# Performance work log

Hardware: AMD Instinct MI355X
Metric: run time of the kernel (lower is better)

The kernel has to match this reference:

```python
import jax, jax.numpy as jnp
import numpy as np

MARGIN = 0.3
EPS = 1e-6  # torch TripletMarginLoss pairwise_distance eps


def setup_inputs() -> dict:
    key = jax.random.key(0)
    k1, k2 = jax.random.split(key)
    n, d = 8192, 128
    inputs = jax.random.normal(k1, (n, d), dtype=jnp.float32)
    similarity = jax.random.randint(k2, (n, n), 0, 2, dtype=jnp.int32)
    return {"inputs": inputs, "similarity": similarity}


def reference(inputs, similarity):
    # mask[i, j] = True if j is a positive of anchor i
    mask = similarity != 0                      # (n, n) bool
    maskf = mask.astype(inputs.dtype)
    counts = maskf.sum(axis=1, keepdims=True)   # (n, 1), >0 by construction
    # per-anchor center = mean of its positives (masked mean as a GEMM)
    centers = (maskf @ inputs) / counts         # (n, d)
    # dist[i, j] = ||centers[i] - inputs[j]||_2 via the expansion trick
    # (avoids materializing the (n, n, d) difference tensor of the original)
    c2 = jnp.sum(centers * centers, axis=1)[:, None]
    x2 = jnp.sum(inputs * inputs, axis=1)[None, :]
    d2 = c2 + x2 - 2.0 * (centers @ inputs.T)
    dist = jnp.sqrt(jnp.maximum(d2, 0.0))       # (n, n)
    # dist only feeds argmin in the original (indices carry no grad)
    dist = jax.lax.stop_gradient(dist)
    # hard-negative mining: argmin of dist over negatives of each anchor
    neg_idx = jnp.argmin(jnp.where(mask, jnp.inf, dist), axis=1)  # (n,)
    neg_min = inputs[neg_idx]                   # (n, d)
    # TripletMarginLoss(margin=0.3, p=2): anchor=centers, pos=inputs, neg=neg_min
    d_ap = jnp.linalg.norm(centers - inputs + EPS, axis=1)
    d_an = jnp.linalg.norm(centers - neg_min + EPS, axis=1)
    return jnp.mean(jnp.maximum(d_ap - d_an + MARGIN, 0.0))
```

## Files before the change

kernel.cpp:

```cpp
#include <hip/hip_runtime.h>
#include <stdint.h>

#define NN 8192
#define DD 128

typedef float f32x4 __attribute__((ext_vector_type(4)));
typedef short bf16x8 __attribute__((ext_vector_type(8)));

union B8 { uint32_t u[4]; bf16x8 v; };

__device__ inline uint16_t f2bf(float f) {
  uint32_t u = __builtin_bit_cast(uint32_t, f);
  uint32_t r = (u + 0x7FFFu + ((u >> 16) & 1u)) >> 16;
  return (uint16_t)r;
}

__device__ inline f32x4 mfma16(bf16x8 a, bf16x8 b, f32x4 c) {
  return __builtin_amdgcn_mfma_f32_16x16x32_bf16(a, b, c, 0, 0, 0);
}

__device__ inline void gl_lds16(const uint16_t* g, uint16_t* l) {
  __builtin_amdgcn_global_load_lds((const __attribute__((address_space(1))) void*)g,
                                   (__attribute__((address_space(3))) void*)l, 16, 0, 0);
}

__global__ __launch_bounds__(256, 2) void k_prep_bitgen(const float* __restrict__ inp,
                                                        const int* __restrict__ sim,
                                                        uint16_t* __restrict__ inp_bf,
                                                        uint16_t* __restrict__ inpT_bf,
                                                        float* __restrict__ x2p,
                                                        uint32_t* __restrict__ bmT,
                                                        uint32_t* __restrict__ negkey,
                                                        uint32_t* __restrict__ sem,
                                                        float* __restrict__ out) {
  __shared__ uint32_t shmem[4416];
  const int tid = threadIdx.x;
  const int bid = blockIdx.x;
  if (bid < 128) {
    uint16_t* ldsT = (uint16_t*)shmem;
    float* ldsS = (float*)(shmem + 4160);
    const int gid = bid * 256 + tid;
    if (gid < NN) negkey[gid] = 0xFFFFFFFFu;
    if (gid < 64) sem[gid] = 0u;
    if (gid == 0) out[0] = 0.f;
    const int j0 = bid * 64;
    const int r = tid >> 2;
    const int dseg = (tid & 3) * 32;
    float ss = 0.f;
#pragma unroll
    for (int it = 0; it < 8; ++it) {
      float4 v = *(const float4*)(inp + (size_t)(j0 + r) * DD + dseg + it * 4);
      ss += v.x * v.x + v.y * v.y + v.z * v.z + v.w * v.w;
      uint16_t b0 = f2bf(v.x), b1 = f2bf(v.y), b2 = f2bf(v.z), b3 = f2bf(v.w);
      *(ushort4*)(inp_bf + (size_t)(j0 + r) * DD + dseg + it * 4) = make_ushort4(b0, b1, b2, b3);
      int d = dseg + it * 4;
      ldsT[(d + 0) * 65 + r] = b0;
      ldsT[(d + 1) * 65 + r] = b1;
      ldsT[(d + 2) * 65 + r] = b2;
      ldsT[(d + 3) * 65 + r] = b3;
    }
    ldsS[tid] = ss;
    __syncthreads();
    if (tid < 64)
      x2p[j0 + tid] = ldsS[tid * 4] + ldsS[tid * 4 + 1] + ldsS[tid * 4 + 2] + ldsS[tid * 4 + 3] + 512.0f;
#pragma unroll
    for (int it = 0; it < 32; ++it) {
      int flat = it * 256 + tid;
      int d = flat >> 6, jl = flat & 63;
      inpT_bf[(size_t)d * NN + j0 + jl] = ldsT[d * 65 + jl];
    }
  } else {
    uint32_t* ldsW = shmem;
    const int bx = bid - 128;
    const int lane = tid & 63, w = tid >> 6;
    const int m0 = (bx & 127) * 64;
    const int c0 = (bx >> 7) * 2048;
    int va[32], vb[32];
    {
      const int* p = sim + (size_t)(m0 + w) * NN + c0 + lane;
#pragma unroll
      for (int s = 0; s < 32; ++s) va[s] = p[s * 64];
    }
#pragma unroll 1
    for (int rr = 0; rr < 16; ++rr) {
      const int rl = rr * 4 + w;
      if (rr < 15) {
        const int* p = sim + (size_t)(m0 + rl + 4) * NN + c0 + lane;
#pragma unroll
        for (int s = 0; s < 32; ++s) vb[s] = p[s * 64];
      }
#pragma unroll
      for (int s = 0; s < 32; ++s) {
        unsigned long long ball = __ballot(va[s] != 0);
        if ((lane & 31) == 0)
          ldsW[(s * 2 + (lane >> 5)) * 64 + rl] = (uint32_t)(ball >> (lane & 32));
      }
#pragma unroll
      for (int s = 0; s < 32; ++s) va[s] = vb[s];
    }
    __syncthreads();
#pragma unroll
    for (int it = 0; it < 16; ++it) {
      int idx = it * 256 + tid;
      int kw = idx >> 6, r = idx & 63;
      bmT[(size_t)((c0 >> 5) + kw) * NN + m0 + r] = ldsW[idx];
    }
  }
}

__global__ __launch_bounds__(256, 2) void k_gemm1(const uint16_t* __restrict__ inpT,
                                                  const uint32_t* __restrict__ bmT,
                                                  float* __restrict__ part,
                                                  uint32_t* __restrict__ sem,
                                                  float* __restrict__ centers,
                                                  uint16_t* __restrict__ cen_bf) {
  __shared__ __align__(16) uint16_t ldsB[2][128 * 64];
  __shared__ float sInv[128];
  __shared__ uint32_t s_done;
  const int tid = threadIdx.x, lane = tid & 63, w = tid >> 6;
  const int col = lane & 15, quad = lane >> 4;
  const int m0 = blockIdx.x * 128;
  const int kb0 = blockIdx.y * 1024;
  const int wm = (w >> 1) * 64, wn = (w & 1) * 64;
  const int swz = (col & 7) << 4;
  f32x4 acc[4][4];
  const f32x4 z = {0.f, 0.f, 0.f, 0.f};
#pragma unroll
  for (int r = 0; r < 4; ++r)
#pragma unroll
    for (int c = 0; c < 4; ++c) acc[r][c] = z;

  uint32_t mwA[8], mwB[8];
  const int srow = lane >> 3;
  const int schk = (lane & 7) ^ (srow & 7);

#define STAGE3(BUF, KB)                                                                       \
  {                                                                                           \
    _Pragma("unroll") for (int c = 0; c < 4; ++c) {                                           \
      const uint16_t* gsrc =                                                                  \
          inpT + (size_t)(w * 32 + c * 8 + srow) * NN + (KB) + (schk << 3);                   \
      gl_lds16(gsrc, &ldsB[BUF][(w * 32 + c * 8) * 64]);                                      \
    }                                                                                         \
  }

#define LDM3(MW, KB)                                                                          \
  {                                                                                           \
    _Pragma("unroll") for (int rr = 0; rr < 4; ++rr)                                          \
      _Pragma("unroll") for (int h = 0; h < 2; ++h)                                           \
        MW[rr * 2 + h] = bmT[(size_t)(((KB) >> 5) + h) * NN + m0 + wm + rr * 16 + col];       \
  }

#define COMP3(BUF, MW)                                                                        \
  {                                                                                           \
    _Pragma("unroll") for (int h = 0; h < 2; ++h) {                                           \
      B8 af[4];                                                                               \
      _Pragma("unroll") for (int rr = 0; rr < 4; ++rr) {                                      \
        uint32_t word = MW[rr * 2 + h];                                                       \
        uint32_t b = (word >> (quad * 8)) & 0xFFu;                                            \
        uint32_t s = b * 0x8001u;                                                             \
        _Pragma("unroll") for (int p = 0; p < 4; ++p)                                         \
          af[rr].u[p] = ((s >> (2 * p)) & 0x10001u) * 0x3F80u;                                \
      }                                                                                       \
      const int eoff = ((h * 64 + quad * 16) ^ swz) >> 1;                                     \
      _Pragma("unroll") for (int cc = 0; cc < 4; ++cc) {                                      \
        bf16x8 bfr = *(const bf16x8*)(&ldsB[BUF][(wn + cc * 16 + col) * 64 + eoff]);          \
        _Pragma("unroll") for (int rr = 0; rr < 4; ++rr)                                      \
          acc[rr][cc] = mfma16(af[rr].v, bfr, acc[rr][cc]);                                   \
      }                                                                                       \
    }                                                                                         \
  }

  STAGE3(0, kb0);
  LDM3(mwA, kb0);
  __syncthreads();
#pragma unroll 1
  for (int ks = 0; ks < 16; ks += 2) {
    const int kb = kb0 + ks * 64;
    STAGE3(1, kb + 64);
    LDM3(mwB, kb + 64);
    COMP3(0, mwA);
    __syncthreads();
    if (ks + 2 < 16) {
      STAGE3(0, kb + 128);
      LDM3(mwA, kb + 128);
    }
    COMP3(1, mwB);
    __syncthreads();
  }
#undef STAGE3
#undef LDM3
#undef COMP3

  float* pp = part + (size_t)blockIdx.y * NN * DD;
#pragma unroll
  for (int rr = 0; rr < 4; ++rr)
#pragma unroll
    for (int cc = 0; cc < 4; ++cc)
#pragma unroll
      for (int g = 0; g < 4; ++g)
        pp[(size_t)(m0 + wm + rr * 16 + quad * 4 + g) * DD + wn + cc * 16 + col] = acc[rr][cc][g];

  __threadfence();
  __syncthreads();
  if (tid == 0) s_done = atomicAdd(&sem[blockIdx.x], 1u);
  __syncthreads();
  if (s_done != 7u) return;
  __threadfence();

  if (tid < 128) {
    uint32_t cnt = 0;
#pragma unroll 4
    for (int kw = 0; kw < 256; ++kw) cnt += __popc(bmT[(size_t)kw * NN + m0 + tid]);
    sInv[tid] = 1.0f / (float)cnt;
  }
  __syncthreads();

#pragma unroll 1
  for (int it = 0; it < 16; ++it) {
    const int f4 = it * 256 + tid;
    const int row = f4 >> 5;
    const int c4 = (f4 & 31) * 4;
    const size_t idx = (size_t)(m0 + row) * DD + c4;
    float4 v = *(const float4*)(part + idx);
#pragma unroll
    for (int s = 1; s < 8; ++s) {
      float4 u = *(const float4*)(part + (size_t)s * NN * DD + idx);
      v.x += u.x; v.y += u.y; v.z += u.z; v.w += u.w;
    }
    const float inv = sInv[row];
    v.x *= inv; v.y *= inv; v.z *= inv; v.w *= inv;
    *(float4*)(centers + idx) = v;
    *(ushort4*)(cen_bf + idx) = make_ushort4(f2bf(v.x), f2bf(v.y), f2bf(v.z), f2bf(v.w));
  }
}

__global__ __launch_bounds__(256, 2) void k_argmin(const uint16_t* __restrict__ cen_bf,
                                                   const uint16_t* __restrict__ inp_bf,
                                                   const uint32_t* __restrict__ bmT,
                                                   const float* __restrict__ x2p,
                                                   uint32_t* __restrict__ negkey) {
  __shared__ __align__(16) uint16_t ldsX[2][64 * 128];
  const int tid = threadIdx.x, lane = tid & 63, w = tid >> 6;
  const int col = lane & 15, quad = lane >> 4;
  const int i0 = blockIdx.x * 128;
  const int jbase = blockIdx.y * 1024;
  const int wi = w * 32;
  const int swz = (col & 7) << 4;

  bf16x8 af[2][4];
#pragma unroll
  for (int rr = 0; rr < 2; ++rr)
#pragma unroll
    for (int kk = 0; kk < 4; ++kk)
      af[rr][kk] = *(const bf16x8*)(cen_bf + (size_t)(i0 + wi + rr * 16 + col) * DD + kk * 32 + quad * 8);

  uint32_t best[2][4];
#pragma unroll
  for (int rr = 0; rr < 2; ++rr)
#pragma unroll
    for (int g = 0; g < 4; ++g) best[rr][g] = 0xFFFFFFFFu;

  const f32x4 z = {0.f, 0.f, 0.f, 0.f};
  const int srow = lane >> 4;

#define STAGE5(BUF, J0)                                                                       \
  {                                                                                           \
    _Pragma("unroll") for (int c = 0; c < 4; ++c) {                                           \
      const int r7 = (c * 4 + srow) & 7;                                                      \
      const uint16_t* gsrc =                                                                  \
          inp_bf + (size_t)((J0) + w * 16 + c * 4 + srow) * DD + (((lane & 15) ^ r7) << 3);   \
      gl_lds16(gsrc, &ldsX[BUF][(w * 16 + c * 4) * 128]);                                     \
    }                                                                                         \
  }

#define COMP5(BUF, J0)                                                                        \
  {                                                                                           \
    uint32_t mw[2][2][4];                                                                     \
    float xv[4];                                                                              \
    _Pragma("unroll") for (int h = 0; h < 2; ++h)                                             \
      _Pragma("unroll") for (int rr = 0; rr < 2; ++rr)                                        \
        _Pragma("unroll") for (int g = 0; g < 4; ++g)                                         \
          mw[h][rr][g] =                                                                      \
              bmT[(size_t)(((J0) >> 5) + h) * NN + i0 + wi + rr * 16 + quad * 4 + g];         \
    _Pragma("unroll") for (int cc = 0; cc < 4; ++cc) xv[cc] = x2p[(J0) + cc * 16 + col];      \
    f32x4 acc[2][4];                                                                          \
    _Pragma("unroll") for (int rr = 0; rr < 2; ++rr)                                          \
      _Pragma("unroll") for (int cc = 0; cc < 4; ++cc) acc[rr][cc] = z;                       \
    _Pragma("unroll") for (int kk = 0; kk < 4; ++kk) {                                        \
      const int eoff = ((kk * 64 + quad * 16) ^ swz) >> 1;                                    \
      _Pragma("unroll") for (int cc = 0; cc < 4; ++cc) {                                      \
        bf16x8 b = *(const bf16x8*)(&ldsX[BUF][(cc * 16 + col) * 128 + eoff]);                \
        acc[0][cc] = mfma16(af[0][kk], b, acc[0][cc]);                                        \
        acc[1][cc] = mfma16(af[1][kk], b, acc[1][cc]);                                        \
      }                                                                                       \
    }                                                                                         \
    _Pragma("unroll") for (int cc = 0; cc < 4; ++cc) {                                        \
      const int jj = cc * 16 + col;                                                           \
      const float xq = xv[cc];                                                                \
      const uint32_t jpre = (uint32_t)((J0) + jj);                                            \
      const int sh = 31 - ((cc & 1) * 16 + col);                                              \
      _Pragma("unroll") for (int rr = 0; rr < 2; ++rr)                                        \
        _Pragma("unroll") for (int g = 0; g < 4; ++g) {                                       \
          float v = fmaf(-2.0f, acc[rr][cc][g], xq);                                          \
          uint32_t u = __builtin_bit_cast(uint32_t, v);                                       \
          uint32_t key = (u & 0xFFFFE000u) | jpre;                                            \
          key |= (mw[cc >> 1][rr][g] << sh) & 0x80000000u;                                    \
          best[rr][g] = min(best[rr][g], key);                                                \
        }                                                                                     \
    }                                                                                         \
  }

  STAGE5(0, jbase);
  __syncthreads();
#pragma unroll 1
  for (int st = 0; st < 16; st += 2) {
    const int j0 = jbase + st * 64;
    STAGE5(1, j0 + 64);
    COMP5(0, j0);
    __syncthreads();
    if (st + 2 < 16) STAGE5(0, j0 + 128);
    COMP5(1, j0 + 64);
    __syncthreads();
  }
#undef STAGE5
#undef COMP5

#pragma unroll
  for (int rr = 0; rr < 2; ++rr)
#pragma unroll
    for (int g = 0; g < 4; ++g) {
      uint32_t k = best[rr][g];
#pragma unroll
      for (int d = 1; d < 16; d <<= 1) {
        uint32_t o = (uint32_t)__shfl_xor((int)k, d);
        k = min(k, o);
      }
      if (col == 0) atomicMin(&negkey[i0 + wi + rr * 16 + quad * 4 + g], k);
    }
}

__global__ __launch_bounds__(256) void k_loss(const float* __restrict__ centers,
                                              const float* __restrict__ inp,
                                              const uint32_t* __restrict__ negkey,
                                              float* __restrict__ out) {
  __shared__ float lds[4];
  const int tid = threadIdx.x, lane = tid & 63, w = tid >> 6;
  float local = 0.f;
#pragma unroll 1
  for (int a = 0; a < 4; ++a) {
    int i = blockIdx.x * 16 + w * 4 + a;
    float2 c = *(const float2*)(centers + (size_t)i * DD + lane * 2);
    float2 x = *(const float2*)(inp + (size_t)i * DD + lane * 2);
    uint32_t ni = negkey[i] & (NN - 1);
    float2 gv = *(const float2*)(inp + (size_t)ni * DD + lane * 2);
    float e0 = c.x - x.x + 1e-6f, e1 = c.y - x.y + 1e-6f;
    float f0 = c.x - gv.x + 1e-6f, f1 = c.y - gv.y + 1e-6f;
    float dap = e0 * e0 + e1 * e1;
    float dan = f0 * f0 + f1 * f1;
#pragma unroll
    for (int d = 32; d; d >>= 1) {
      dap += __shfl_down(dap, d);
      dan += __shfl_down(dan, d);
    }
    if (lane == 0) local += fmaxf(sqrtf(dap) - sqrtf(dan) + 0.3f, 0.f);
  }
  if (lane == 0) lds[w] = local;
  __syncthreads();
  if (tid == 0) atomicAdd(out, (lds[0] + lds[1] + lds[2] + lds[3]) * (1.0f / 8192.0f));
}

extern "C" void kernel_launch(void* const* d_in, const int* in_sizes, int n_in,
                              void* d_out, int out_size, void* d_ws, size_t ws_size,
                              hipStream_t stream) {
  (void)in_sizes; (void)n_in; (void)out_size; (void)ws_size;
  const float* inp = (const float*)d_in[0];
  const int* sim = (const int*)d_in[1];
  float* out = (float*)d_out;
  char* ws = (char*)d_ws;

  uint32_t* bmT     = (uint32_t*)ws;
  float* part       = (float*)(ws + (8u << 20));
  float* centers    = (float*)(ws + (40u << 20));
  uint16_t* inp_bf  = (uint16_t*)(ws + (44u << 20));
  uint16_t* inpT_bf = (uint16_t*)(ws + (46u << 20));
  uint16_t* cen_bf  = (uint16_t*)(ws + (48u << 20));
  float* x2p        = (float*)(ws + (50u << 20));
  uint32_t* sem     = (uint32_t*)(ws + (50u << 20) + 32768u);
  uint32_t* negkey  = (uint32_t*)(ws + (50u << 20) + 65536u);

  k_prep_bitgen<<<640, 256, 0, stream>>>(inp, sim, inp_bf, inpT_bf, x2p, bmT, negkey, sem, out);
  k_gemm1<<<dim3(64, 8), 256, 0, stream>>>(inpT_bf, bmT, part, sem, centers, cen_bf);
  k_argmin<<<dim3(64, 8), 256, 0, stream>>>(cen_bf, inp_bf, bmT, x2p, negkey);
  k_loss<<<512, 256, 0, stream>>>(centers, inp, negkey, out);
}
```

Before: 518.6 us.

## Fuse all stages into one persistent kernel with software grid barriers

Merges the prep/bitgen, masked GEMM, center reduction, argmin and loss kernels into a single 512-block kernel separated by atomic-counter grid barriers. Per-row positive counts are now gathered with popcount atomics during bitmask generation, and the reduction of the partial center sums is spread across all blocks instead of only the last block per row tile. The aim is to remove kernel launch gaps and the serialized tail reduction. In exchange it adds spin-wait barrier cost and two memset launches, and it depends on all 512 blocks being co-resident (2 per CU) to avoid deadlock.

```diff
diff --git a/kernel.cpp b/kernel.cpp
--- a/kernel.cpp
+++ b/kernel.cpp
@@ -3,6 +3,7 @@
 
 #define NN 8192
 #define DD 128
+#define GRID 512
 
 typedef float f32x4 __attribute__((ext_vector_type(4)));
 typedef short bf16x8 __attribute__((ext_vector_type(8)));
@@ -24,24 +25,41 @@
                                    (__attribute__((address_space(3))) void*)l, 16, 0, 0);
 }
 
-__global__ __launch_bounds__(256, 2) void k_prep_bitgen(const float* __restrict__ inp,
-                                                        const int* __restrict__ sim,
-                                                        uint16_t* __restrict__ inp_bf,
-                                                        uint16_t* __restrict__ inpT_bf,
-                                                        float* __restrict__ x2p,
-                                                        uint32_t* __restrict__ bmT,
-                                                        uint32_t* __restrict__ negkey,
-                                                        uint32_t* __restrict__ sem,
-                                                        float* __restrict__ out) {
-  __shared__ uint32_t shmem[4416];
+__device__ inline void gbar(uint32_t* cnt, uint32_t tgt) {
+  __syncthreads();
+  __threadfence();
+  if (threadIdx.x == 0) {
+    atomicAdd(cnt, 1u);
+    while (atomicAdd(cnt, 0u) < tgt) __builtin_amdgcn_s_sleep(8);
+  }
+  __syncthreads();
+  __threadfence();
+}
+
+__global__ __launch_bounds__(256, 2) void k_mega(const float* __restrict__ inp,
+                                                 const int* __restrict__ sim,
+                                                 uint16_t* __restrict__ inp_bf,
+                                                 uint16_t* __restrict__ inpT_bf,
+                                                 float* __restrict__ x2p,
+                                                 uint32_t* __restrict__ bmT,
+                                                 uint32_t* __restrict__ counts,
+                                                 float* __restrict__ part,
+                                                 float* __restrict__ centers,
+                                                 uint16_t* __restrict__ cen_bf,
+                                                 uint32_t* __restrict__ negkey,
+                                                 float* __restrict__ out,
+                                                 uint32_t* __restrict__ bar) {
+  __shared__ __align__(16) uint8_t smem[32768];
   const int tid = threadIdx.x;
   const int bid = blockIdx.x;
+  const int lane = tid & 63, w = tid >> 6;
+  const int col = lane & 15, quad = lane >> 4;
+
   if (bid < 128) {
-    uint16_t* ldsT = (uint16_t*)shmem;
-    float* ldsS = (float*)(shmem + 4160);
+    uint16_t* ldsT = (uint16_t*)smem;
+    float* ldsS = (float*)(smem + 16640);
     const int gid = bid * 256 + tid;
     if (gid < NN) negkey[gid] = 0xFFFFFFFFu;
-    if (gid < 64) sem[gid] = 0u;
     if (gid == 0) out[0] = 0.f;
     const int j0 = bid * 64;
     const int r = tid >> 2;
@@ -69,12 +87,12 @@
       int d = flat >> 6, jl = flat & 63;
       inpT_bf[(size_t)d * NN + j0 + jl] = ldsT[d * 65 + jl];
     }
-  } else {
-    uint32_t* ldsW = shmem;
-    const int bx = bid - 128;
-    const int lane = tid & 63, w = tid >> 6;
-    const int m0 = (bx & 127) * 64;
-    const int c0 = (bx >> 7) * 2048;
+    __syncthreads();
+  }
+  {
+    uint32_t* ldsW = (uint32_t*)smem;
+    const int m0 = (bid & 127) * 64;
+    const int c0 = (bid >> 7) * 2048;
     int va[32], vb[32];
     {
       const int* p = sim + (size_t)(m0 + w) * NN + c0 + lane;
@@ -89,12 +107,15 @@
 #pragma unroll
         for (int s = 0; s < 32; ++s) vb[s] = p[s * 64];
       }
+      uint32_t cnt = 0;
 #pragma unroll
       for (int s = 0; s < 32; ++s) {
         unsigned long long ball = __ballot(va[s] != 0);
+        cnt += (uint32_t)__popcll(ball);
         if ((lane & 31) == 0)
           ldsW[(s * 2 + (lane >> 5)) * 64 + rl] = (uint32_t)(ball >> (lane & 32));
       }
+      if (lane == 0) atomicAdd(&counts[m0 + rl], cnt);
 #pragma unroll
       for (int s = 0; s < 32; ++s) va[s] = vb[s];
     }
@@ -106,39 +127,31 @@
       bmT[(size_t)((c0 >> 5) + kw) * NN + m0 + r] = ldsW[idx];
     }
   }
-}
-
-__global__ __launch_bounds__(256, 2) void k_gemm1(const uint16_t* __restrict__ inpT,
-                                                  const uint32_t* __restrict__ bmT,
-                                                  float* __restrict__ part,
-                                                  uint32_t* __restrict__ sem,
-                                                  float* __restrict__ centers,
-                                                  uint16_t* __restrict__ cen_bf) {
-  __shared__ __align__(16) uint16_t ldsB[2][128 * 64];
-  __shared__ float sInv[128];
-  __shared__ uint32_t s_done;
-  const int tid = threadIdx.x, lane = tid & 63, w = tid >> 6;
-  const int col = lane & 15, quad = lane >> 4;
-  const int m0 = blockIdx.x * 128;
-  const int kb0 = blockIdx.y * 1024;
-  const int wm = (w >> 1) * 64, wn = (w & 1) * 64;
-  const int swz = (col & 7) << 4;
-  f32x4 acc[4][4];
-  const f32x4 z = {0.f, 0.f, 0.f, 0.f};
-#pragma unroll
-  for (int r = 0; r < 4; ++r)
-#pragma unroll
-    for (int c = 0; c < 4; ++c) acc[r][c] = z;
-
-  uint32_t mwA[8], mwB[8];
-  const int srow = lane >> 3;
-  const int schk = (lane & 7) ^ (srow & 7);
+  gbar(bar, 1 * GRID);
+
+  {
+    uint16_t (*ldsB)[128 * 64] = (uint16_t(*)[128 * 64])smem;
+    const int bx = bid & 63, by = bid >> 6;
+    const int m0 = bx * 128;
+    const int kb0 = by * 1024;
+    const int wm = (w >> 1) * 64, wn = (w & 1) * 64;
+    const int swz = (col & 7) << 4;
+    f32x4 acc[4][4];
+    const f32x4 z = {0.f, 0.f, 0.f, 0.f};
+#pragma unroll
+    for (int r = 0; r < 4; ++r)
+#pragma unroll
+      for (int c = 0; c < 4; ++c) acc[r][c] = z;
+
+    uint32_t mwA[8], mwB[8];
+    const int srow = lane >> 3;
+    const int schk = (lane & 7) ^ (srow & 7);
 
 #define STAGE3(BUF, KB)                                                                       \
   {                                                                                           \
     _Pragma("unroll") for (int c = 0; c < 4; ++c) {                                           \
       const uint16_t* gsrc =                                                                  \
-          inpT + (size_t)(w * 32 + c * 8 + srow) * NN + (KB) + (schk << 3);                   \
+          inpT_bf + (size_t)(w * 32 + c * 8 + srow) * NN + (KB) + (schk << 3);                \
       gl_lds16(gsrc, &ldsB[BUF][(w * 32 + c * 8) * 64]);                                      \
     }                                                                                         \
   }
@@ -170,98 +183,81 @@
     }                                                                                         \
   }
 
-  STAGE3(0, kb0);
-  LDM3(mwA, kb0);
-  __syncthreads();
-#pragma unroll 1
-  for (int ks = 0; ks < 16; ks += 2) {
-    const int kb = kb0 + ks * 64;
-    STAGE3(1, kb + 64);
-    LDM3(mwB, kb + 64);
-    COMP3(0, mwA);
-    __syncthreads();
-    if (ks + 2 < 16) {
-      STAGE3(0, kb + 128);
-      LDM3(mwA, kb + 128);
-    }
-    COMP3(1, mwB);
-    __syncthreads();
-  }
+    STAGE3(0, kb0);
+    LDM3(mwA, kb0);
+    __syncthreads();
+#pragma unroll 1
+    for (int ks = 0; ks < 16; ks += 2) {
+      const int kb = kb0 + ks * 64;
+      STAGE3(1, kb + 64);
+      LDM3(mwB, kb + 64);
+      COMP3(0, mwA);
+      __syncthreads();
+      if (ks + 2 < 16) {
+        STAGE3(0, kb + 128);
+        LDM3(mwA, kb + 128);
+      }
+      COMP3(1, mwB);
+      __syncthreads();
+    }
 #undef STAGE3
 #undef LDM3
 #undef COMP3
 
-  float* pp = part + (size_t)blockIdx.y * NN * DD;
-#pragma unroll
-  for (int rr = 0; rr < 4; ++rr)
-#pragma unroll
-    for (int cc = 0; cc < 4; ++cc)
-#pragma unroll
-      for (int g = 0; g < 4; ++g)
-        pp[(size_t)(m0 + wm + rr * 16 + quad * 4 + g) * DD + wn + cc * 16 + col] = acc[rr][cc][g];
-
-  __threadfence();
-  __syncthreads();
-  if (tid == 0) s_done = atomicAdd(&sem[blockIdx.x], 1u);
-  __syncthreads();
-  if (s_done != 7u) return;
-  __threadfence();
-
-  if (tid < 128) {
-    uint32_t cnt = 0;
-#pragma unroll 4
-    for (int kw = 0; kw < 256; ++kw) cnt += __popc(bmT[(size_t)kw * NN + m0 + tid]);
-    sInv[tid] = 1.0f / (float)cnt;
-  }
-  __syncthreads();
-
-#pragma unroll 1
-  for (int it = 0; it < 16; ++it) {
-    const int f4 = it * 256 + tid;
-    const int row = f4 >> 5;
-    const int c4 = (f4 & 31) * 4;
-    const size_t idx = (size_t)(m0 + row) * DD + c4;
-    float4 v = *(const float4*)(part + idx);
-#pragma unroll
-    for (int s = 1; s < 8; ++s) {
-      float4 u = *(const float4*)(part + (size_t)s * NN * DD + idx);
-      v.x += u.x; v.y += u.y; v.z += u.z; v.w += u.w;
-    }
-    const float inv = sInv[row];
-    v.x *= inv; v.y *= inv; v.z *= inv; v.w *= inv;
-    *(float4*)(centers + idx) = v;
-    *(ushort4*)(cen_bf + idx) = make_ushort4(f2bf(v.x), f2bf(v.y), f2bf(v.z), f2bf(v.w));
-  }
-}
-
-__global__ __launch_bounds__(256, 2) void k_argmin(const uint16_t* __restrict__ cen_bf,
-                                                   const uint16_t* __restrict__ inp_bf,
-                                                   const uint32_t* __restrict__ bmT,
-                                                   const float* __restrict__ x2p,
-                                                   uint32_t* __restrict__ negkey) {
-  __shared__ __align__(16) uint16_t ldsX[2][64 * 128];
-  const int tid = threadIdx.x, lane = tid & 63, w = tid >> 6;
-  const int col = lane & 15, quad = lane >> 4;
-  const int i0 = blockIdx.x * 128;
-  const int jbase = blockIdx.y * 1024;
-  const int wi = w * 32;
-  const int swz = (col & 7) << 4;
-
-  bf16x8 af[2][4];
-#pragma unroll
-  for (int rr = 0; rr < 2; ++rr)
-#pragma unroll
-    for (int kk = 0; kk < 4; ++kk)
-      af[rr][kk] = *(const bf16x8*)(cen_bf + (size_t)(i0 + wi + rr * 16 + col) * DD + kk * 32 + quad * 8);
-
-  uint32_t best[2][4];
-#pragma unroll
-  for (int rr = 0; rr < 2; ++rr)
-#pragma unroll
-    for (int g = 0; g < 4; ++g) best[rr][g] = 0xFFFFFFFFu;
-
-  const f32x4 z = {0.f, 0.f, 0.f, 0.f};
-  const int srow = lane >> 4;
+    float* pp = part + (size_t)by * NN * DD;
+#pragma unroll
+    for (int rr = 0; rr < 4; ++rr)
+#pragma unroll
+      for (int cc = 0; cc < 4; ++cc)
+#pragma unroll
+        for (int g = 0; g < 4; ++g)
+          pp[(size_t)(m0 + wm + rr * 16 + quad * 4 + g) * DD + wn + cc * 16 + col] = acc[rr][cc][g];
+  }
+  gbar(bar, 2 * GRID);
+
+  {
+#pragma unroll 1
+    for (int rep = 0; rep < 2; ++rep) {
+      const int fg = rep * 131072 + bid * 256 + tid;
+      const int idx = fg * 4;
+      const int row = idx >> 7;
+      const float inv = 1.0f / (float)counts[row];
+      float4 v = *(const float4*)(part + idx);
+#pragma unroll
+      for (int s = 1; s < 8; ++s) {
+        float4 u = *(const float4*)(part + (size_t)s * NN * DD + idx);
+        v.x += u.x; v.y += u.y; v.z += u.z; v.w += u.w;
+      }
+      v.x *= inv; v.y *= inv; v.z *= inv; v.w *= inv;
+      *(float4*)(centers + idx) = v;
+      *(ushort4*)(cen_bf + idx) = make_ushort4(f2bf(v.x), f2bf(v.y), f2bf(v.z), f2bf(v.w));
+    }
+  }
+  gbar(bar, 3 * GRID);
+
+  {
+    uint16_t (*ldsX)[64 * 128] = (uint16_t(*)[64 * 128])smem;
+    const int bx = bid & 63, by = bid >> 6;
+    const int i0 = bx * 128;
+    const int jbase = by * 1024;
+    const int wi = w * 32;
+    const int swz = (col & 7) << 4;
+
+    bf16x8 af[2][4];
+#pragma unroll
+    for (int rr = 0; rr < 2; ++rr)
+#pragma unroll
+      for (int kk = 0; kk < 4; ++kk)
+        af[rr][kk] = *(const bf16x8*)(cen_bf + (size_t)(i0 + wi + rr * 16 + col) * DD + kk * 32 + quad * 8);
+
+    uint32_t best[2][4];
+#pragma unroll
+    for (int rr = 0; rr < 2; ++rr)
+#pragma unroll
+      for (int g = 0; g < 4; ++g) best[rr][g] = 0xFFFFFFFFu;
+
+    const f32x4 z = {0.f, 0.f, 0.f, 0.f};
+    const int srow = lane >> 4;
 
 #define STAGE5(BUF, J0)                                                                       \
   {                                                                                           \
@@ -310,63 +306,61 @@
     }                                                                                         \
   }
 
-  STAGE5(0, jbase);
-  __syncthreads();
-#pragma unroll 1
-  for (int st = 0; st < 16; st += 2) {
-    const int j0 = jbase + st * 64;
-    STAGE5(1, j0 + 64);
-    COMP5(0, j0);
-    __syncthreads();
-    if (st + 2 < 16) STAGE5(0, j0 + 128);
-    COMP5(1, j0 + 64);
-    __syncthreads();
-  }
+    STAGE5(0, jbase);
+    __syncthreads();
+#pragma unroll 1
+    for (int st = 0; st < 16; st += 2) {
+      const int j0 = jbase + st * 64;
+      STAGE5(1, j0 + 64);
+      COMP5(0, j0);
+      __syncthreads();
+      if (st + 2 < 16) STAGE5(0, j0 + 128);
+      COMP5(1, j0 + 64);
+      __syncthreads();
+    }
 #undef STAGE5
 #undef COMP5
 
 #pragma unroll
-  for (int rr = 0; rr < 2; ++rr)
-#pragma unroll
-    for (int g = 0; g < 4; ++g) {
-      uint32_t k = best[rr][g];
-#pragma unroll
-      for (int d = 1; d < 16; d <<= 1) {
-        uint32_t o = (uint32_t)__shfl_xor((int)k, d);
-        k = min(k, o);
-      }
-      if (col == 0) atomicMin(&negkey[i0 + wi + rr * 16 + quad * 4 + g], k);
-    }
-}
-
-__global__ __launch_bounds__(256) void k_loss(const float* __restrict__ centers,
-                                              const float* __restrict__ inp,
-                                              const uint32_t* __restrict__ negkey,
-                                              float* __restrict__ out) {
-  __shared__ float lds[4];
-  const int tid = threadIdx.x, lane = tid & 63, w = tid >> 6;
-  float local = 0.f;
-#pragma unroll 1
-  for (int a = 0; a < 4; ++a) {
-    int i = blockIdx.x * 16 + w * 4 + a;
-    float2 c = *(const float2*)(centers + (size_t)i * DD + lane * 2);
-    float2 x = *(const float2*)(inp + (size_t)i * DD + lane * 2);
-    uint32_t ni = negkey[i] & (NN - 1);
-    float2 gv = *(const float2*)(inp + (size_t)ni * DD + lane * 2);
-    float e0 = c.x - x.x + 1e-6f, e1 = c.y - x.y + 1e-6f;
-    float f0 = c.x - gv.x + 1e-6f, f1 = c.y - gv.y + 1e-6f;
-    float dap = e0 * e0 + e1 * e1;
-    float dan = f0 * f0 + f1 * f1;
-#pragma unroll
-    for (int d = 32; d; d >>= 1) {
-      dap += __shfl_down(dap, d);
-      dan += __shfl_down(dan, d);
-    }
-    if (lane == 0) local += fmaxf(sqrtf(dap) - sqrtf(dan) + 0.3f, 0.f);
-  }
-  if (lane == 0) lds[w] = local;
-  __syncthreads();
-  if (tid == 0) atomicAdd(out, (lds[0] + lds[1] + lds[2] + lds[3]) * (1.0f / 8192.0f));
+    for (int rr = 0; rr < 2; ++rr)
+#pragma unroll
+      for (int g = 0; g < 4; ++g) {
+        uint32_t k = best[rr][g];
+#pragma unroll
+        for (int d = 1; d < 16; d <<= 1) {
+          uint32_t o = (uint32_t)__shfl_xor((int)k, d);
+          k = min(k, o);
+        }
+        if (col == 0) atomicMin(&negkey[i0 + wi + rr * 16 + quad * 4 + g], k);
+      }
+  }
+  gbar(bar, 4 * GRID);
+
+  {
+    float* ldsL = (float*)smem;
+    float local = 0.f;
+#pragma unroll 1
+    for (int a = 0; a < 4; ++a) {
+      int i = bid * 16 + w * 4 + a;
+      float2 c = *(const float2*)(centers + (size_t)i * DD + lane * 2);
+      float2 x = *(const float2*)(inp + (size_t)i * DD + lane * 2);
+      uint32_t ni = negkey[i] & (NN - 1);
+      float2 gv = *(const float2*)(inp + (size_t)ni * DD + lane * 2);
+      float e0 = c.x - x.x + 1e-6f, e1 = c.y - x.y + 1e-6f;
+      float f0 = c.x - gv.x + 1e-6f, f1 = c.y - gv.y + 1e-6f;
+      float dap = e0 * e0 + e1 * e1;
+      float dan = f0 * f0 + f1 * f1;
+#pragma unroll
+      for (int d = 32; d; d >>= 1) {
+        dap += __shfl_down(dap, d);
+        dan += __shfl_down(dan, d);
+      }
+      if (lane == 0) local += fmaxf(sqrtf(dap) - sqrtf(dan) + 0.3f, 0.f);
+    }
+    if (lane == 0) ldsL[w] = local;
+    __syncthreads();
+    if (tid == 0) atomicAdd(out, (ldsL[0] + ldsL[1] + ldsL[2] + ldsL[3]) * (1.0f / 8192.0f));
+  }
 }
 
 extern "C" void kernel_launch(void* const* d_in, const int* in_sizes, int n_in,
@@ -385,11 +379,12 @@
   uint16_t* inpT_bf = (uint16_t*)(ws + (46u << 20));
   uint16_t* cen_bf  = (uint16_t*)(ws + (48u << 20));
   float* x2p        = (float*)(ws + (50u << 20));
-  uint32_t* sem     = (uint32_t*)(ws + (50u << 20) + 32768u);
+  uint32_t* counts  = (uint32_t*)(ws + (50u << 20) + 32768u);
   uint32_t* negkey  = (uint32_t*)(ws + (50u << 20) + 65536u);
-
-  k_prep_bitgen<<<640, 256, 0, stream>>>(inp, sim, inp_bf, inpT_bf, x2p, bmT, negkey, sem, out);
-  k_gemm1<<<dim3(64, 8), 256, 0, stream>>>(inpT_bf, bmT, part, sem, centers, cen_bf);
-  k_argmin<<<dim3(64, 8), 256, 0, stream>>>(cen_bf, inp_bf, bmT, x2p, negkey);
-  k_loss<<<512, 256, 0, stream>>>(centers, inp, negkey, out);
-}
+  uint32_t* bar     = (uint32_t*)(ws + (50u << 20) + 98304u);
+
+  hipMemsetAsync(counts, 0, 32768, stream);
+  hipMemsetAsync(bar, 0, 64, stream);
+  k_mega<<<GRID, 256, 0, stream>>>(inp, sim, inp_bf, inpT_bf, x2p, bmT, counts, part,
+                                   centers, cen_bf, negkey, out, bar);
+}
```

New measurement: 886.3 us. 1.71x slower.

## Split split-K reduction into separate kernel and compute counts during bitmask generation

Applied to the files above, without the earlier changes.

Removes the last-block semaphore pattern in the GEMM kernel, where the eighth finishing block for each row tile serially reduced eight partial slices and re-scanned the bitmask to count positives. Per-row positive counts are now accumulated with popcount during bitmask generation, written per column slice, and a new fully parallel reduce kernel sums partials and normalizes. This spreads the reduction across all CUs instead of 64 tail blocks, at the cost of an extra kernel launch and a small counts buffer.

```diff
diff --git a/kernel.cpp b/kernel.cpp
--- a/kernel.cpp
+++ b/kernel.cpp
@@ -30,8 +30,8 @@
                                                         uint16_t* __restrict__ inpT_bf,
                                                         float* __restrict__ x2p,
                                                         uint32_t* __restrict__ bmT,
+                                                        uint32_t* __restrict__ counts4,
                                                         uint32_t* __restrict__ negkey,
-                                                        uint32_t* __restrict__ sem,
                                                         float* __restrict__ out) {
   __shared__ uint32_t shmem[4416];
   const int tid = threadIdx.x;
@@ -41,7 +41,6 @@
     float* ldsS = (float*)(shmem + 4160);
     const int gid = bid * 256 + tid;
     if (gid < NN) negkey[gid] = 0xFFFFFFFFu;
-    if (gid < 64) sem[gid] = 0u;
     if (gid == 0) out[0] = 0.f;
     const int j0 = bid * 64;
     const int r = tid >> 2;
@@ -75,6 +74,7 @@
     const int lane = tid & 63, w = tid >> 6;
     const int m0 = (bx & 127) * 64;
     const int c0 = (bx >> 7) * 2048;
+    const int slice = bx >> 7;
     int va[32], vb[32];
     {
       const int* p = sim + (size_t)(m0 + w) * NN + c0 + lane;
@@ -89,12 +89,15 @@
 #pragma unroll
         for (int s = 0; s < 32; ++s) vb[s] = p[s * 64];
       }
+      uint32_t cnt = 0;
 #pragma unroll
       for (int s = 0; s < 32; ++s) {
         unsigned long long ball = __ballot(va[s] != 0);
+        cnt += (uint32_t)__popcll(ball);
         if ((lane & 31) == 0)
           ldsW[(s * 2 + (lane >> 5)) * 64 + rl] = (uint32_t)(ball >> (lane & 32));
       }
+      if (lane == 0) counts4[(size_t)slice * NN + m0 + rl] = cnt;
 #pragma unroll
       for (int s = 0; s < 32; ++s) va[s] = vb[s];
     }
@@ -110,13 +113,8 @@
 
 __global__ __launch_bounds__(256, 2) void k_gemm1(const uint16_t* __restrict__ inpT,
                                                   const uint32_t* __restrict__ bmT,
-                                                  float* __restrict__ part,
-                                                  uint32_t* __restrict__ sem,
-                                                  float* __restrict__ centers,
-                                                  uint16_t* __restrict__ cen_bf) {
+                                                  float* __restrict__ part) {
   __shared__ __align__(16) uint16_t ldsB[2][128 * 64];
-  __shared__ float sInv[128];
-  __shared__ uint32_t s_done;
   const int tid = threadIdx.x, lane = tid & 63, w = tid >> 6;
   const int col = lane & 15, quad = lane >> 4;
   const int m0 = blockIdx.x * 128;
@@ -199,39 +197,26 @@
 #pragma unroll
       for (int g = 0; g < 4; ++g)
         pp[(size_t)(m0 + wm + rr * 16 + quad * 4 + g) * DD + wn + cc * 16 + col] = acc[rr][cc][g];
-
-  __threadfence();
-  __syncthreads();
-  if (tid == 0) s_done = atomicAdd(&sem[blockIdx.x], 1u);
-  __syncthreads();
-  if (s_done != 7u) return;
-  __threadfence();
-
-  if (tid < 128) {
-    uint32_t cnt = 0;
-#pragma unroll 4
-    for (int kw = 0; kw < 256; ++kw) cnt += __popc(bmT[(size_t)kw * NN + m0 + tid]);
-    sInv[tid] = 1.0f / (float)cnt;
-  }
-  __syncthreads();
-
-#pragma unroll 1
-  for (int it = 0; it < 16; ++it) {
-    const int f4 = it * 256 + tid;
-    const int row = f4 >> 5;
-    const int c4 = (f4 & 31) * 4;
-    const size_t idx = (size_t)(m0 + row) * DD + c4;
-    float4 v = *(const float4*)(part + idx);
-#pragma unroll
-    for (int s = 1; s < 8; ++s) {
-      float4 u = *(const float4*)(part + (size_t)s * NN * DD + idx);
-      v.x += u.x; v.y += u.y; v.z += u.z; v.w += u.w;
-    }
-    const float inv = sInv[row];
-    v.x *= inv; v.y *= inv; v.z *= inv; v.w *= inv;
-    *(float4*)(centers + idx) = v;
-    *(ushort4*)(cen_bf + idx) = make_ushort4(f2bf(v.x), f2bf(v.y), f2bf(v.z), f2bf(v.w));
-  }
+}
+
+__global__ __launch_bounds__(256) void k_reduce(const float* __restrict__ part,
+                                                const uint32_t* __restrict__ counts4,
+                                                float* __restrict__ centers,
+                                                uint16_t* __restrict__ cen_bf) {
+  const int gid = blockIdx.x * 256 + threadIdx.x;
+  const int idx = gid * 4;
+  const int row = idx >> 7;
+  const uint32_t cnt = counts4[row] + counts4[NN + row] + counts4[2 * NN + row] + counts4[3 * NN + row];
+  const float inv = 1.0f / (float)cnt;
+  float4 v = *(const float4*)(part + idx);
+#pragma unroll
+  for (int s = 1; s < 8; ++s) {
+    float4 u = *(const float4*)(part + (size_t)s * NN * DD + idx);
+    v.x += u.x; v.y += u.y; v.z += u.z; v.w += u.w;
+  }
+  v.x *= inv; v.y *= inv; v.z *= inv; v.w *= inv;
+  *(float4*)(centers + idx) = v;
+  *(ushort4*)(cen_bf + idx) = make_ushort4(f2bf(v.x), f2bf(v.y), f2bf(v.z), f2bf(v.w));
 }
 
 __global__ __launch_bounds__(256, 2) void k_argmin(const uint16_t* __restrict__ cen_bf,
@@ -385,11 +370,12 @@
   uint16_t* inpT_bf = (uint16_t*)(ws + (46u << 20));
   uint16_t* cen_bf  = (uint16_t*)(ws + (48u << 20));
   float* x2p        = (float*)(ws + (50u << 20));
-  uint32_t* sem     = (uint32_t*)(ws + (50u << 20) + 32768u);
-  uint32_t* negkey  = (uint32_t*)(ws + (50u << 20) + 65536u);
-
-  k_prep_bitgen<<<640, 256, 0, stream>>>(inp, sim, inp_bf, inpT_bf, x2p, bmT, negkey, sem, out);
-  k_gemm1<<<dim3(64, 8), 256, 0, stream>>>(inpT_bf, bmT, part, sem, centers, cen_bf);
+  uint32_t* counts4 = (uint32_t*)(ws + (50u << 20) + 32768u);
+  uint32_t* negkey  = (uint32_t*)(ws + (50u << 20) + 196608u);
+
+  k_prep_bitgen<<<640, 256, 0, stream>>>(inp, sim, inp_bf, inpT_bf, x2p, bmT, counts4, negkey, out);
+  k_gemm1<<<dim3(64, 8), 256, 0, stream>>>(inpT_bf, bmT, part);
+  k_reduce<<<1024, 256, 0, stream>>>(part, counts4, centers, cen_bf);
   k_argmin<<<dim3(64, 8), 256, 0, stream>>>(cen_bf, inp_bf, bmT, x2p, negkey);
   k_loss<<<512, 256, 0, stream>>>(centers, inp, negkey, out);
 }
```

After: 440.7 us. 1.18x faster.
